# Performance work log

Hardware: AMD Instinct MI355X
Metric: run time of the kernel (lower is better)

The kernel has to match this reference:

```python
import jax, jax.numpy as jnp
import numpy as np

N, F_IN, H, F_OUT = 8192, 256, 128, 16
POOL_RATIO = 0.5


def setup_inputs() -> dict:
    key = jax.random.key(0)
    ks = jax.random.split(key, 12)
    # Sparse-ish symmetric adjacency with zero diagonal (avg degree ~32).
    A = (jax.random.uniform(ks[0], (N, N)) < (32.0 / N)).astype(jnp.float32)
    A = jnp.maximum(A, A.T) * (1.0 - jnp.eye(N, dtype=jnp.float32))
    x = jax.random.normal(ks[1], (N, F_IN), dtype=jnp.float32)

    def lin(k, fin, fout):
        return (jax.random.normal(k, (fin, fout), dtype=jnp.float32) / np.float32(np.sqrt(fin)))

    return {
        "x": x, "A": A,
        "W0": lin(ks[2], F_IN, H), "b0": jnp.zeros((H,), jnp.float32),
        "W1": lin(ks[3], H, H),    "b1": jnp.zeros((H,), jnp.float32),
        "pw": lin(ks[4], H, 1),    "pb": jnp.zeros((1,), jnp.float32),
        "Wu": lin(ks[5], H, H),    "bu": jnp.zeros((H,), jnp.float32),
        "Wf": lin(ks[6], H, F_OUT), "bf": jnp.zeros((F_OUT,), jnp.float32),
    }


def _norm_adj(A):
    # normalize(): add self-loops (diag of A is 0), row-normalize D^-1 (A+I)
    Ah = A + jnp.eye(A.shape[0], dtype=A.dtype)
    r = jnp.sum(Ah, axis=1)
    r_inv = jnp.where(r > 0, 1.0 / r, 0.0)
    return Ah * r_inv[:, None]


def _gconv(x, A, W, b, act):
    h = x @ W + b          # nn.Linear
    h = _norm_adj(A) @ h   # spmm with row-normalized adjacency
    return act(h)


def reference(x, A, W0, b0, W1, b1, pw, pb, Wu, bu, Wf, bf):
    relu = jax.nn.relu
    ident = lambda t: t
    # down gconv 0
    h0 = _gconv(x, A, W0, b0, relu)                       # [N, H]
    # gPool: score -> l2-normalize -> sigmoid -> top-k gather
    score = h0 @ pw + pb                                  # [N, 1]
    score = score / jnp.sqrt(jnp.sum(score ** 2))
    score = jax.nn.sigmoid(score[:, 0])                   # [N]
    k = max(2, int(POOL_RATIO * h0.shape[0]))
    vals, idx = jax.lax.top_k(score, k)                   # [k]
    xp = h0[idx] * vals[:, None]                          # gated gather [k, H]
    Ap = A[idx][:, idx]                                   # pooled adjacency [k, k]
    # down gconv 1 (bottleneck, no pool after)
    h1 = _gconv(xp, Ap, W1, b1, relu)                     # [k, H]
    # gUnpool: zero-scatter back to N nodes
    xu = jnp.zeros((A.shape[0], h1.shape[1]), h1.dtype).at[idx].set(h1)
    # up gconv
    hu = _gconv(xu, A, Wu, bu, relu)                      # [N, H]
    # final gconv (identity activation) + log_softmax
    hf = _gconv(hu, A, Wf, bf, ident)                     # [N, F_OUT]
    return jax.nn.log_softmax(hf, axis=1)
```

## Files before the change

### kernel.cpp

```cpp
#include <hip/hip_runtime.h>
#include <math.h>

#define N_NODES 8192
#define FIN 256
#define HDIM 128
#define FOUTD 16
#define KSEL 4096
#define CAP 256

__global__ void build_csr(const float* __restrict__ A, int* __restrict__ cols,
                          int* __restrict__ deg) {
    int row = blockIdx.x;
    __shared__ int cnt;
    __shared__ int scols[CAP];
    if (threadIdx.x == 0) cnt = 0;
    __syncthreads();
    const float4* Arow = (const float4*)(A + (size_t)row * N_NODES);
    for (int c4 = threadIdx.x; c4 < N_NODES / 4; c4 += blockDim.x) {
        float4 v = Arow[c4];
        int base = c4 * 4;
        if (v.x != 0.0f) { int p = atomicAdd(&cnt, 1); if (p < CAP) scols[p] = base; }
        if (v.y != 0.0f) { int p = atomicAdd(&cnt, 1); if (p < CAP) scols[p] = base + 1; }
        if (v.z != 0.0f) { int p = atomicAdd(&cnt, 1); if (p < CAP) scols[p] = base + 2; }
        if (v.w != 0.0f) { int p = atomicAdd(&cnt, 1); if (p < CAP) scols[p] = base + 3; }
    }
    __syncthreads();
    int c = cnt; if (c > CAP) c = CAP;
    for (int i = threadIdx.x; i < c; i += blockDim.x)
        cols[(size_t)row * CAP + i] = scols[i];
    if (threadIdx.x == 0) deg[row] = c;
}

template <int FI>
__global__ void gemm128(const float* __restrict__ X, const float* __restrict__ W,
                        const float* __restrict__ b, const float* __restrict__ scale,
                        float* __restrict__ Y) {
    __shared__ float Xs[8][FI];
    int tid = threadIdx.x;
    int row0 = blockIdx.x * 8;
    for (int i = tid; i < 8 * FI; i += 128) {
        int r = i / FI, k = i - r * FI;
        float v = X[(size_t)(row0 + r) * FI + k];
        if (scale) v *= scale[row0 + r];
        Xs[r][k] = v;
    }
    __syncthreads();
    float acc[8];
    float bias = b[tid];
#pragma unroll
    for (int r = 0; r < 8; r++) acc[r] = bias;
    for (int k = 0; k < FI; k++) {
        float w = W[k * HDIM + tid];
#pragma unroll
        for (int r = 0; r < 8; r++) acc[r] = fmaf(Xs[r][k], w, acc[r]);
    }
#pragma unroll
    for (int r = 0; r < 8; r++) Y[(size_t)(row0 + r) * HDIM + tid] = acc[r];
}

__global__ void gemm16(const float* __restrict__ X, const float* __restrict__ W,
                       const float* __restrict__ b, float* __restrict__ Y) {
    __shared__ float Xs[16][HDIM + 1];
    __shared__ float Ws[HDIM * FOUTD];
    int tid = threadIdx.x;
    int row0 = blockIdx.x * 16;
    for (int i = tid; i < 16 * HDIM; i += 256) {
        int r = i / HDIM, k = i - r * HDIM;
        Xs[r][k] = X[(size_t)(row0 + r) * HDIM + k];
    }
    for (int i = tid; i < HDIM * FOUTD; i += 256) Ws[i] = W[i];
    __syncthreads();
    int c = tid & 15, r = tid >> 4;
    float acc = b[c];
    for (int k = 0; k < HDIM; k++) acc = fmaf(Xs[r][k], Ws[k * FOUTD + c], acc);
    Y[(size_t)(row0 + r) * FOUTD + c] = acc;
}

__global__ void spmm128_full(const float* __restrict__ T, const int* __restrict__ cols,
                             const int* __restrict__ deg, float* __restrict__ OUT,
                             int relu) {
    int row = blockIdx.x;
    int lane = threadIdx.x;
    const int* cl = cols + (size_t)row * CAP;
    int d = deg[row];
    float a0 = 0.f, a1 = 0.f, a2 = 0.f, a3 = 0.f;
    int j = 0;
    for (; j + 4 <= d; j += 4) {
        int c0 = cl[j], c1 = cl[j + 1], c2 = cl[j + 2], c3 = cl[j + 3];
        a0 += T[(size_t)c0 * HDIM + lane];
        a1 += T[(size_t)c1 * HDIM + lane];
        a2 += T[(size_t)c2 * HDIM + lane];
        a3 += T[(size_t)c3 * HDIM + lane];
    }
    for (; j < d; j++) a0 += T[(size_t)cl[j] * HDIM + lane];
    float acc = T[(size_t)row * HDIM + lane] + ((a0 + a1) + (a2 + a3));
    float v = acc / (float)(1 + d);
    if (relu) v = fmaxf(v, 0.f);
    OUT[(size_t)row * HDIM + lane] = v;
}

__global__ void spmm128_pool(const float* __restrict__ T, const int* __restrict__ cols,
                             const int* __restrict__ deg, const int* __restrict__ sel,
                             float* __restrict__ OUT) {
    int row = blockIdx.x;
    int lane = threadIdx.x;
    if (!sel[row]) { OUT[(size_t)row * HDIM + lane] = 0.f; return; }
    const int* cl = cols + (size_t)row * CAP;
    int d = deg[row];
    float acc = T[(size_t)row * HDIM + lane];
    int cnt = 0;
    for (int j = 0; j < d; j++) {
        int c = cl[j];
        if (sel[c]) { cnt++; acc += T[(size_t)c * HDIM + lane]; }
    }
    float v = acc / (float)(1 + cnt);
    OUT[(size_t)row * HDIM + lane] = fmaxf(v, 0.f);
}

__global__ void score_k(const float* __restrict__ H0, const float* __restrict__ pw,
                        const float* __restrict__ pb, float* __restrict__ sraw) {
    int wave = threadIdx.x >> 6, lane = threadIdx.x & 63;
    int row = blockIdx.x * 4 + wave;
    float v = H0[(size_t)row * HDIM + lane] * pw[lane] +
              H0[(size_t)row * HDIM + lane + 64] * pw[lane + 64];
    for (int off = 32; off; off >>= 1) v += __shfl_down(v, off);
    if (lane == 0) sraw[row] = v + pb[0];
}

__global__ void __launch_bounds__(1024) topk_kernel(const float* __restrict__ sraw,
                                                    int* __restrict__ sel,
                                                    float* __restrict__ g) {
    int tid = threadIdx.x;
    float v[8];
    unsigned key[8];
    float ss = 0.f;
#pragma unroll
    for (int e = 0; e < 8; e++) {
        float x = sraw[tid * 8 + e];
        v[e] = x;
        ss += x * x;
        unsigned b = __float_as_uint(x);
        key[e] = (b & 0x80000000u) ? ~b : (b | 0x80000000u);
    }
    __shared__ float fred[16];
    __shared__ int ired[16];
    __shared__ float bc_f;
    __shared__ int bc_i;
    for (int off = 32; off; off >>= 1) ss += __shfl_down(ss, off);
    if ((tid & 63) == 0) fred[tid >> 6] = ss;
    __syncthreads();
    if (tid == 0) { float t = 0; for (int i = 0; i < 16; i++) t += fred[i]; bc_f = t; }
    __syncthreads();
    float inv_norm = 1.0f / sqrtf(bc_f);

    unsigned lo = 0u, hi = 0xFFFFFFFFu;
    while (lo < hi) {
        unsigned mid = lo + ((hi - lo) >> 1) + 1u;
        int c = 0;
#pragma unroll
        for (int e = 0; e < 8; e++) c += (key[e] >= mid);
        for (int off = 32; off; off >>= 1) c += __shfl_down(c, off);
        if ((tid & 63) == 0) ired[tid >> 6] = c;
        __syncthreads();
        if (tid == 0) { int t = 0; for (int i = 0; i < 16; i++) t += ired[i]; bc_i = t; }
        __syncthreads();
        if (bc_i >= KSEL) lo = mid; else hi = mid - 1u;
        __syncthreads();
    }
    unsigned T = lo;
    int cg = 0;
#pragma unroll
    for (int e = 0; e < 8; e++) cg += (key[e] > T);
    for (int off = 32; off; off >>= 1) cg += __shfl_down(cg, off);
    if ((tid & 63) == 0) ired[tid >> 6] = cg;
    __syncthreads();
    if (tid == 0) { int t = 0; for (int i = 0; i < 16; i++) t += ired[i]; bc_i = t; }
    __syncthreads();
    int need = KSEL - bc_i;
    int eq = 0;
#pragma unroll
    for (int e = 0; e < 8; e++) eq += (key[e] == T);
    __shared__ int sc[1024];
    sc[tid] = eq;
    __syncthreads();
    for (int off = 1; off < 1024; off <<= 1) {
        int val = (tid >= off) ? sc[tid - off] : 0;
        __syncthreads();
        sc[tid] += val;
        __syncthreads();
    }
    int excl = sc[tid] - eq;
    int seen = 0;
#pragma unroll
    for (int e = 0; e < 8; e++) {
        int i = tid * 8 + e;
        int s;
        if (key[e] > T) s = 1;
        else if (key[e] == T) { s = (excl + seen < need) ? 1 : 0; seen++; }
        else s = 0;
        sel[i] = s;
        g[i] = s ? (1.0f / (1.0f + expf(-(v[e] * inv_norm)))) : 0.0f;
    }
}

__global__ void spmm16_lsm(const float* __restrict__ T3, const int* __restrict__ cols,
                           const int* __restrict__ deg, float* __restrict__ out) {
    int lane = threadIdx.x;
    int r = lane >> 4, c = lane & 15;
    int row = blockIdx.x * 4 + r;
    const int* cl = cols + (size_t)row * CAP;
    int d = deg[row];
    float acc = T3[(size_t)row * FOUTD + c];
    for (int j = 0; j < d; j++) acc += T3[(size_t)cl[j] * FOUTD + c];
    float v = acc / (float)(1 + d);
    float m = v;
    for (int off = 1; off < 16; off <<= 1) m = fmaxf(m, __shfl_xor(m, off, 16));
    float e = expf(v - m);
    float s = e;
    for (int off = 1; off < 16; off <<= 1) s += __shfl_xor(s, off, 16);
    out[(size_t)row * FOUTD + c] = v - m - logf(s);
}

extern "C" void kernel_launch(void* const* d_in, const int* in_sizes, int n_in,
                              void* d_out, int out_size, void* d_ws, size_t ws_size,
                              hipStream_t stream) {
    const float* x  = (const float*)d_in[0];
    const float* A  = (const float*)d_in[1];
    const float* W0 = (const float*)d_in[2];
    const float* b0 = (const float*)d_in[3];
    const float* W1 = (const float*)d_in[4];
    const float* b1 = (const float*)d_in[5];
    const float* pw = (const float*)d_in[6];
    const float* pb = (const float*)d_in[7];
    const float* Wu = (const float*)d_in[8];
    const float* bu = (const float*)d_in[9];
    const float* Wf = (const float*)d_in[10];
    const float* bf = (const float*)d_in[11];
    float* out = (float*)d_out;

    char* ws = (char*)d_ws;
    int*   cols = (int*)  (ws);
    int*   deg  = (int*)  (ws + 8388608);
    float* T    = (float*)(ws + 8421376);
    float* H0   = (float*)(ws + 12615680);
    float* XU   = (float*)(ws + 16809984);
    float* T3   = (float*)(ws + 21004288);
    float* sraw = (float*)(ws + 21528576);
    int*   sel  = (int*)  (ws + 21561344);
    float* g    = (float*)(ws + 21594112);

    build_csr<<<N_NODES, 256, 0, stream>>>(A, cols, deg);
    gemm128<FIN><<<N_NODES / 8, 128, 0, stream>>>(x, W0, b0, nullptr, T);
    spmm128_full<<<N_NODES, 128, 0, stream>>>(T, cols, deg, H0, 1);
    score_k<<<N_NODES / 4, 256, 0, stream>>>(H0, pw, pb, sraw);
    topk_kernel<<<1, 1024, 0, stream>>>(sraw, sel, g);
    gemm128<HDIM><<<N_NODES / 8, 128, 0, stream>>>(H0, W1, b1, g, T);
    spmm128_pool<<<N_NODES, 128, 0, stream>>>(T, cols, deg, sel, XU);
    gemm128<HDIM><<<N_NODES / 8, 128, 0, stream>>>(XU, Wu, bu, nullptr, T);
    spmm128_full<<<N_NODES, 128, 0, stream>>>(T, cols, deg, H0, 1);
    gemm16<<<N_NODES / 16, 256, 0, stream>>>(H0, Wf, bf, T3);
    spmm16_lsm<<<N_NODES / 4, 64, 0, stream>>>(T3, cols, deg, out);
}
```

Baseline: 605.8 us.

## Fuse score into spmm, radix top-k, bf16 intermediates, fuse spmm with following GEMMs

```diff
diff --git a/kernel.cpp b/kernel.cpp
--- a/kernel.cpp
+++ b/kernel.cpp
@@ -6,10 +6,21 @@
 #define HDIM 128
 #define FOUTD 16
 #define KSEL 4096
-#define CAP 256
-
-__global__ void build_csr(const float* __restrict__ A, int* __restrict__ cols,
-                          int* __restrict__ deg) {
+#define CAP 128
+
+typedef unsigned int uint;
+typedef unsigned short ushort;
+
+static __device__ __forceinline__ ushort f2bf(float f) {
+    uint u = __float_as_uint(f);
+    return (ushort)((u + 0x7FFFu + ((u >> 16) & 1u)) >> 16);
+}
+static __device__ __forceinline__ float bf_lo(uint u) { return __uint_as_float(u << 16); }
+static __device__ __forceinline__ float bf_hi(uint u) { return __uint_as_float(u & 0xFFFF0000u); }
+
+__global__ __launch_bounds__(256) void build_csr(const float* __restrict__ A,
+                                                 int* __restrict__ cols,
+                                                 int* __restrict__ deg) {
     int row = blockIdx.x;
     __shared__ int cnt;
     __shared__ int scols[CAP];
@@ -31,54 +42,49 @@
     if (threadIdx.x == 0) deg[row] = c;
 }
 
-template <int FI>
-__global__ void gemm128(const float* __restrict__ X, const float* __restrict__ W,
-                        const float* __restrict__ b, const float* __restrict__ scale,
-                        float* __restrict__ Y) {
-    __shared__ float Xs[8][FI];
+template <int FI, int OUT_BF16>
+__global__ __launch_bounds__(128) void gemm_t(const float* __restrict__ X,
+                                              const float* __restrict__ W,
+                                              const float* __restrict__ b,
+                                              const float* __restrict__ scale,
+                                              void* __restrict__ Y) {
     int tid = threadIdx.x;
     int row0 = blockIdx.x * 8;
-    for (int i = tid; i < 8 * FI; i += 128) {
-        int r = i / FI, k = i - r * FI;
-        float v = X[(size_t)(row0 + r) * FI + k];
-        if (scale) v *= scale[row0 + r];
-        Xs[r][k] = v;
-    }
-    __syncthreads();
     float acc[8];
+#pragma unroll
+    for (int r = 0; r < 8; r++) acc[r] = 0.0f;
+    const float* Xb = X + (size_t)row0 * FI;
+    for (int k = 0; k < FI; k += 4) {
+        float w0 = W[(k + 0) * HDIM + tid];
+        float w1 = W[(k + 1) * HDIM + tid];
+        float w2 = W[(k + 2) * HDIM + tid];
+        float w3 = W[(k + 3) * HDIM + tid];
+#pragma unroll
+        for (int r = 0; r < 8; r++) {
+            const float* xr = Xb + r * FI + k;
+            acc[r] = fmaf(xr[0], w0, acc[r]);
+            acc[r] = fmaf(xr[1], w1, acc[r]);
+            acc[r] = fmaf(xr[2], w2, acc[r]);
+            acc[r] = fmaf(xr[3], w3, acc[r]);
+        }
+    }
     float bias = b[tid];
 #pragma unroll
-    for (int r = 0; r < 8; r++) acc[r] = bias;
-    for (int k = 0; k < FI; k++) {
-        float w = W[k * HDIM + tid];
-#pragma unroll
-        for (int r = 0; r < 8; r++) acc[r] = fmaf(Xs[r][k], w, acc[r]);
-    }
-#pragma unroll
-    for (int r = 0; r < 8; r++) Y[(size_t)(row0 + r) * HDIM + tid] = acc[r];
-}
-
-__global__ void gemm16(const float* __restrict__ X, const float* __restrict__ W,
-                       const float* __restrict__ b, float* __restrict__ Y) {
-    __shared__ float Xs[16][HDIM + 1];
-    __shared__ float Ws[HDIM * FOUTD];
-    int tid = threadIdx.x;
-    int row0 = blockIdx.x * 16;
-    for (int i = tid; i < 16 * HDIM; i += 256) {
-        int r = i / HDIM, k = i - r * HDIM;
-        Xs[r][k] = X[(size_t)(row0 + r) * HDIM + k];
-    }
-    for (int i = tid; i < HDIM * FOUTD; i += 256) Ws[i] = W[i];
-    __syncthreads();
-    int c = tid & 15, r = tid >> 4;
-    float acc = b[c];
-    for (int k = 0; k < HDIM; k++) acc = fmaf(Xs[r][k], Ws[k * FOUTD + c], acc);
-    Y[(size_t)(row0 + r) * FOUTD + c] = acc;
-}
-
-__global__ void spmm128_full(const float* __restrict__ T, const int* __restrict__ cols,
-                             const int* __restrict__ deg, float* __restrict__ OUT,
-                             int relu) {
+    for (int r = 0; r < 8; r++) {
+        float sc = scale ? scale[row0 + r] : 1.0f;
+        float val = fmaf(acc[r], sc, bias);
+        if (OUT_BF16) ((ushort*)Y)[(size_t)(row0 + r) * HDIM + tid] = f2bf(val);
+        else          ((float*)Y)[(size_t)(row0 + r) * HDIM + tid] = val;
+    }
+}
+
+__global__ __launch_bounds__(128) void spmm_score(const float* __restrict__ T0,
+                                                  const int* __restrict__ cols,
+                                                  const int* __restrict__ deg,
+                                                  const float* __restrict__ pw,
+                                                  const float* __restrict__ pb,
+                                                  float* __restrict__ H0,
+                                                  float* __restrict__ sraw) {
     int row = blockIdx.x;
     int lane = threadIdx.x;
     const int* cl = cols + (size_t)row * CAP;
@@ -87,124 +93,185 @@
     int j = 0;
     for (; j + 4 <= d; j += 4) {
         int c0 = cl[j], c1 = cl[j + 1], c2 = cl[j + 2], c3 = cl[j + 3];
-        a0 += T[(size_t)c0 * HDIM + lane];
-        a1 += T[(size_t)c1 * HDIM + lane];
-        a2 += T[(size_t)c2 * HDIM + lane];
-        a3 += T[(size_t)c3 * HDIM + lane];
-    }
-    for (; j < d; j++) a0 += T[(size_t)cl[j] * HDIM + lane];
-    float acc = T[(size_t)row * HDIM + lane] + ((a0 + a1) + (a2 + a3));
-    float v = acc / (float)(1 + d);
-    if (relu) v = fmaxf(v, 0.f);
-    OUT[(size_t)row * HDIM + lane] = v;
-}
-
-__global__ void spmm128_pool(const float* __restrict__ T, const int* __restrict__ cols,
-                             const int* __restrict__ deg, const int* __restrict__ sel,
-                             float* __restrict__ OUT) {
+        a0 += T0[(size_t)c0 * HDIM + lane];
+        a1 += T0[(size_t)c1 * HDIM + lane];
+        a2 += T0[(size_t)c2 * HDIM + lane];
+        a3 += T0[(size_t)c3 * HDIM + lane];
+    }
+    for (; j < d; j++) a0 += T0[(size_t)cl[j] * HDIM + lane];
+    float acc = T0[(size_t)row * HDIM + lane] + ((a0 + a1) + (a2 + a3));
+    float h = fmaxf(acc / (float)(1 + d), 0.f);
+    H0[(size_t)row * HDIM + lane] = h;
+    float v = h * pw[lane];
+    for (int off = 32; off; off >>= 1) v += __shfl_down(v, off);
+    __shared__ float ws2[2];
+    if ((lane & 63) == 0) ws2[lane >> 6] = v;
+    __syncthreads();
+    if (lane == 0) sraw[row] = ws2[0] + ws2[1] + pb[0];
+}
+
+__global__ __launch_bounds__(256) void topk_radix(const float* __restrict__ sraw,
+                                                  int* __restrict__ sel,
+                                                  float* __restrict__ g) {
+    int tid = threadIdx.x;
+    float v[32];
+    unsigned key[32];
+    float ss = 0.f;
+#pragma unroll
+    for (int e = 0; e < 32; e++) {
+        float x = sraw[tid * 32 + e];
+        v[e] = x; ss += x * x;
+        unsigned b = __float_as_uint(x);
+        key[e] = (b & 0x80000000u) ? ~b : (b | 0x80000000u);
+    }
+    __shared__ float fr[4];
+    __shared__ float bss;
+    for (int off = 32; off; off >>= 1) ss += __shfl_down(ss, off);
+    if ((tid & 63) == 0) fr[tid >> 6] = ss;
+    __syncthreads();
+    if (tid == 0) bss = fr[0] + fr[1] + fr[2] + fr[3];
+    __syncthreads();
+    float inv_norm = 1.0f / sqrtf(bss);
+
+    __shared__ int hist[256];
+    __shared__ int sfx[256];
+    __shared__ int bd, bkneed;
+    unsigned prefix = 0; int kneed = KSEL;
+    for (int pass = 0; pass < 4; pass++) {
+        int shift = 24 - 8 * pass;
+        unsigned maskAbove = (pass == 0) ? 0u : (0xFFFFFFFFu << (shift + 8));
+        hist[tid] = 0;
+        __syncthreads();
+#pragma unroll
+        for (int e = 0; e < 32; e++)
+            if ((key[e] & maskAbove) == prefix)
+                atomicAdd(&hist[(key[e] >> shift) & 255], 1);
+        __syncthreads();
+        sfx[tid] = hist[tid];
+        __syncthreads();
+        for (int off = 1; off < 256; off <<= 1) {
+            int add = (tid + off < 256) ? sfx[tid + off] : 0;
+            __syncthreads();
+            sfx[tid] += add;
+            __syncthreads();
+        }
+        int s_here = sfx[tid];
+        int s_next = (tid < 255) ? sfx[tid + 1] : 0;
+        if (s_here >= kneed && s_next < kneed) { bd = tid; bkneed = kneed - s_next; }
+        __syncthreads();
+        prefix |= ((unsigned)bd) << shift;
+        kneed = bkneed;
+        __syncthreads();
+    }
+    unsigned T = prefix;
+    int eq = 0;
+#pragma unroll
+    for (int e = 0; e < 32; e++) eq += (key[e] == T);
+    __shared__ int sc[256];
+    sc[tid] = eq;
+    __syncthreads();
+    for (int off = 1; off < 256; off <<= 1) {
+        int add = (tid >= off) ? sc[tid - off] : 0;
+        __syncthreads();
+        sc[tid] += add;
+        __syncthreads();
+    }
+    int excl = sc[tid] - eq;
+    int seen = 0;
+#pragma unroll
+    for (int e = 0; e < 32; e++) {
+        int i = tid * 32 + e;
+        int s;
+        if (key[e] > T) s = 1;
+        else if (key[e] == T) { s = (excl + seen < kneed) ? 1 : 0; seen++; }
+        else s = 0;
+        sel[i] = s;
+        g[i] = s ? (1.0f / (1.0f + expf(-(v[e] * inv_norm)))) : 0.0f;
+    }
+}
+
+__global__ __launch_bounds__(64) void pool_gemm(const uint* __restrict__ T1u,
+                                                const int* __restrict__ cols,
+                                                const int* __restrict__ deg,
+                                                const int* __restrict__ sel,
+                                                const float* __restrict__ Wu,
+                                                const float* __restrict__ bu,
+                                                uint* __restrict__ T2u) {
     int row = blockIdx.x;
-    int lane = threadIdx.x;
-    if (!sel[row]) { OUT[(size_t)row * HDIM + lane] = 0.f; return; }
+    int t = threadIdx.x;
+    float2 bias = ((const float2*)bu)[t];
+    if (!sel[row]) {
+        T2u[(size_t)row * 64 + t] = (uint)f2bf(bias.x) | ((uint)f2bf(bias.y) << 16);
+        return;
+    }
     const int* cl = cols + (size_t)row * CAP;
     int d = deg[row];
-    float acc = T[(size_t)row * HDIM + lane];
+    uint su = T1u[(size_t)row * 64 + t];
+    float ax = bf_lo(su), ay = bf_hi(su);
     int cnt = 0;
     for (int j = 0; j < d; j++) {
         int c = cl[j];
-        if (sel[c]) { cnt++; acc += T[(size_t)c * HDIM + lane]; }
-    }
-    float v = acc / (float)(1 + cnt);
-    OUT[(size_t)row * HDIM + lane] = fmaxf(v, 0.f);
-}
-
-__global__ void score_k(const float* __restrict__ H0, const float* __restrict__ pw,
-                        const float* __restrict__ pb, float* __restrict__ sraw) {
-    int wave = threadIdx.x >> 6, lane = threadIdx.x & 63;
-    int row = blockIdx.x * 4 + wave;
-    float v = H0[(size_t)row * HDIM + lane] * pw[lane] +
-              H0[(size_t)row * HDIM + lane + 64] * pw[lane + 64];
-    for (int off = 32; off; off >>= 1) v += __shfl_down(v, off);
-    if (lane == 0) sraw[row] = v + pb[0];
-}
-
-__global__ void __launch_bounds__(1024) topk_kernel(const float* __restrict__ sraw,
-                                                    int* __restrict__ sel,
-                                                    float* __restrict__ g) {
-    int tid = threadIdx.x;
-    float v[8];
-    unsigned key[8];
-    float ss = 0.f;
-#pragma unroll
-    for (int e = 0; e < 8; e++) {
-        float x = sraw[tid * 8 + e];
-        v[e] = x;
-        ss += x * x;
-        unsigned b = __float_as_uint(x);
-        key[e] = (b & 0x80000000u) ? ~b : (b | 0x80000000u);
-    }
-    __shared__ float fred[16];
-    __shared__ int ired[16];
-    __shared__ float bc_f;
-    __shared__ int bc_i;
-    for (int off = 32; off; off >>= 1) ss += __shfl_down(ss, off);
-    if ((tid & 63) == 0) fred[tid >> 6] = ss;
-    __syncthreads();
-    if (tid == 0) { float t = 0; for (int i = 0; i < 16; i++) t += fred[i]; bc_f = t; }
-    __syncthreads();
-    float inv_norm = 1.0f / sqrtf(bc_f);
-
-    unsigned lo = 0u, hi = 0xFFFFFFFFu;
-    while (lo < hi) {
-        unsigned mid = lo + ((hi - lo) >> 1) + 1u;
-        int c = 0;
-#pragma unroll
-        for (int e = 0; e < 8; e++) c += (key[e] >= mid);
-        for (int off = 32; off; off >>= 1) c += __shfl_down(c, off);
-        if ((tid & 63) == 0) ired[tid >> 6] = c;
-        __syncthreads();
-        if (tid == 0) { int t = 0; for (int i = 0; i < 16; i++) t += ired[i]; bc_i = t; }
-        __syncthreads();
-        if (bc_i >= KSEL) lo = mid; else hi = mid - 1u;
-        __syncthreads();
-    }
-    unsigned T = lo;
-    int cg = 0;
-#pragma unroll
-    for (int e = 0; e < 8; e++) cg += (key[e] > T);
-    for (int off = 32; off; off >>= 1) cg += __shfl_down(cg, off);
-    if ((tid & 63) == 0) ired[tid >> 6] = cg;
-    __syncthreads();
-    if (tid == 0) { int t = 0; for (int i = 0; i < 16; i++) t += ired[i]; bc_i = t; }
-    __syncthreads();
-    int need = KSEL - bc_i;
-    int eq = 0;
-#pragma unroll
-    for (int e = 0; e < 8; e++) eq += (key[e] == T);
-    __shared__ int sc[1024];
-    sc[tid] = eq;
-    __syncthreads();
-    for (int off = 1; off < 1024; off <<= 1) {
-        int val = (tid >= off) ? sc[tid - off] : 0;
-        __syncthreads();
-        sc[tid] += val;
-        __syncthreads();
-    }
-    int excl = sc[tid] - eq;
-    int seen = 0;
-#pragma unroll
-    for (int e = 0; e < 8; e++) {
-        int i = tid * 8 + e;
-        int s;
-        if (key[e] > T) s = 1;
-        else if (key[e] == T) { s = (excl + seen < need) ? 1 : 0; seen++; }
-        else s = 0;
-        sel[i] = s;
-        g[i] = s ? (1.0f / (1.0f + expf(-(v[e] * inv_norm)))) : 0.0f;
-    }
-}
-
-__global__ void spmm16_lsm(const float* __restrict__ T3, const int* __restrict__ cols,
-                           const int* __restrict__ deg, float* __restrict__ out) {
+        if (sel[c]) {
+            cnt++;
+            uint u = T1u[(size_t)c * 64 + t];
+            ax += bf_lo(u); ay += bf_hi(u);
+        }
+    }
+    float inv = 1.0f / (float)(1 + cnt);
+    float xux = fmaxf(ax * inv, 0.f);
+    float xuy = fmaxf(ay * inv, 0.f);
+    float accx = bias.x, accy = bias.y;
+    const float2* Wur = (const float2*)Wu;
+#pragma unroll 4
+    for (int kk = 0; kk < 64; kk++) {
+        float xk0 = __uint_as_float(__builtin_amdgcn_readlane(__float_as_uint(xux), kk));
+        float xk1 = __uint_as_float(__builtin_amdgcn_readlane(__float_as_uint(xuy), kk));
+        float2 w0 = Wur[(size_t)(2 * kk) * 64 + t];
+        float2 w1 = Wur[(size_t)(2 * kk + 1) * 64 + t];
+        accx = fmaf(xk0, w0.x, accx); accy = fmaf(xk0, w0.y, accy);
+        accx = fmaf(xk1, w1.x, accx); accy = fmaf(xk1, w1.y, accy);
+    }
+    T2u[(size_t)row * 64 + t] = (uint)f2bf(accx) | ((uint)f2bf(accy) << 16);
+}
+
+__global__ __launch_bounds__(64) void up_gemm16(const uint* __restrict__ T2u,
+                                                const int* __restrict__ cols,
+                                                const int* __restrict__ deg,
+                                                const float* __restrict__ Wf,
+                                                const float* __restrict__ bf_,
+                                                float* __restrict__ T3) {
+    int row = blockIdx.x;
+    int t = threadIdx.x;
+    const int* cl = cols + (size_t)row * CAP;
+    int d = deg[row];
+    uint su = T2u[(size_t)row * 64 + t];
+    float ax = bf_lo(su), ay = bf_hi(su);
+    for (int j = 0; j < d; j++) {
+        uint u = T2u[(size_t)cl[j] * 64 + t];
+        ax += bf_lo(u); ay += bf_hi(u);
+    }
+    float inv = 1.0f / (float)(1 + d);
+    float hux = fmaxf(ax * inv, 0.f);
+    float huy = fmaxf(ay * inv, 0.f);
+    __shared__ float hs[128];
+    hs[2 * t] = hux; hs[2 * t + 1] = huy;
+    __syncthreads();
+    int c = t & 15, gg = t >> 4;
+    float p = 0.f;
+#pragma unroll 8
+    for (int kk = 0; kk < 32; kk++) {
+        int k = gg * 32 + kk;
+        p = fmaf(hs[k], Wf[k * FOUTD + c], p);
+    }
+    p += __shfl_xor(p, 16);
+    p += __shfl_xor(p, 32);
+    if (t < 16) T3[(size_t)row * FOUTD + t] = p + bf_[t];
+}
+
+__global__ __launch_bounds__(64) void spmm16_lsm(const float* __restrict__ T3,
+                                                 const int* __restrict__ cols,
+                                                 const int* __restrict__ deg,
+                                                 float* __restrict__ out) {
     int lane = threadIdx.x;
     int r = lane >> 4, c = lane & 15;
     int row = blockIdx.x * 4 + r;
@@ -239,25 +306,24 @@
     float* out = (float*)d_out;
 
     char* ws = (char*)d_ws;
+    const size_t MB = 1024 * 1024;
     int*   cols = (int*)  (ws);
-    int*   deg  = (int*)  (ws + 8388608);
-    float* T    = (float*)(ws + 8421376);
-    float* H0   = (float*)(ws + 12615680);
-    float* XU   = (float*)(ws + 16809984);
-    float* T3   = (float*)(ws + 21004288);
-    float* sraw = (float*)(ws + 21528576);
-    int*   sel  = (int*)  (ws + 21561344);
-    float* g    = (float*)(ws + 21594112);
+    int*   deg  = (int*)  (ws + 4  * MB);
+    float* T0   = (float*)(ws + 5  * MB);
+    float* H0   = (float*)(ws + 9  * MB);
+    uint*  T1   = (uint*) (ws + 13 * MB);
+    uint*  T2   = (uint*) (ws + 15 * MB);
+    float* T3   = (float*)(ws + 17 * MB);
+    float* sraw = (float*)(ws + 18 * MB);
+    int*   sel  = (int*)  (ws + 18 * MB + 512 * 1024);
+    float* g    = (float*)(ws + 19 * MB);
 
     build_csr<<<N_NODES, 256, 0, stream>>>(A, cols, deg);
-    gemm128<FIN><<<N_NODES / 8, 128, 0, stream>>>(x, W0, b0, nullptr, T);
-    spmm128_full<<<N_NODES, 128, 0, stream>>>(T, cols, deg, H0, 1);
-    score_k<<<N_NODES / 4, 256, 0, stream>>>(H0, pw, pb, sraw);
-    topk_kernel<<<1, 1024, 0, stream>>>(sraw, sel, g);
-    gemm128<HDIM><<<N_NODES / 8, 128, 0, stream>>>(H0, W1, b1, g, T);
-    spmm128_pool<<<N_NODES, 128, 0, stream>>>(T, cols, deg, sel, XU);
-    gemm128<HDIM><<<N_NODES / 8, 128, 0, stream>>>(XU, Wu, bu, nullptr, T);
-    spmm128_full<<<N_NODES, 128, 0, stream>>>(T, cols, deg, H0, 1);
-    gemm16<<<N_NODES / 16, 256, 0, stream>>>(H0, Wf, bf, T3);
+    gemm_t<FIN, 0><<<N_NODES / 8, 128, 0, stream>>>(x, W0, b0, nullptr, T0);
+    spmm_score<<<N_NODES, 128, 0, stream>>>(T0, cols, deg, pw, pb, H0, sraw);
+    topk_radix<<<1, 256, 0, stream>>>(sraw, sel, g);
+    gemm_t<HDIM, 1><<<N_NODES / 8, 128, 0, stream>>>(H0, W1, b1, g, (void*)T1);
+    pool_gemm<<<N_NODES, 64, 0, stream>>>(T1, cols, deg, sel, Wu, bu, T2);
+    up_gemm16<<<N_NODES, 64, 0, stream>>>(T2, cols, deg, Wf, bf, T3);
     spmm16_lsm<<<N_NODES / 4, 64, 0, stream>>>(T3, cols, deg, out);
 }
```

Result: no change. 594.5 us (-1.9%).
